# Optimization experiments

Hardware: AMD Instinct MI355X
Metric: run time of the kernel (lower is better)

## Reference

```python
import jax, jax.numpy as jnp
import numpy as np

N_NODES = 50000
D_FEAT = 128
N_EDGES = 600000
HIDDEN_1 = 128
HIDDEN_2 = 64


def setup_inputs() -> dict:
    key = jax.random.key(0)
    ks = jax.random.split(key, 8)
    features = jax.random.normal(ks[0], (N_NODES, D_FEAT), dtype=jnp.float32)
    edges = jax.random.randint(ks[1], (N_EDGES, 2), 0, N_NODES, dtype=jnp.int64)
    s1 = 1.0 / np.sqrt(D_FEAT)
    s2 = 1.0 / np.sqrt(2 * HIDDEN_1)
    s3 = 1.0 / np.sqrt(HIDDEN_2)
    return {
        "features": features,
        "edges": edges,
        "W_nb": jax.random.normal(ks[2], (D_FEAT, HIDDEN_1), dtype=jnp.float32) * s1,
        "b_nb": jnp.zeros((HIDDEN_1,), dtype=jnp.float32),
        "W_self": jax.random.normal(ks[3], (D_FEAT, HIDDEN_1), dtype=jnp.float32) * s1,
        "b_self": jnp.zeros((HIDDEN_1,), dtype=jnp.float32),
        "W_att1": jax.random.normal(ks[4], (2 * HIDDEN_1, HIDDEN_2), dtype=jnp.float32) * s2,
        "b_att1": jnp.zeros((HIDDEN_2,), dtype=jnp.float32),
        "W_att2": jax.random.normal(ks[5], (HIDDEN_2, 1), dtype=jnp.float32) * s3,
        "b_att2": jnp.zeros((1,), dtype=jnp.float32),
    }


def reference(features, edges, W_nb, b_nb, W_self, b_self, W_att1, b_att1, W_att2, b_att2):
    # gather endpoint node features for each edge: [E, D_FEAT]
    f1 = features[edges[:, 0]]
    f2 = features[edges[:, 1]]
    # per-endpoint dense projections with relu (inference: no dropout)
    h1 = jax.nn.relu(f1 @ W_nb + b_nb)      # [E, H1]
    h2 = jax.nn.relu(f2 @ W_self + b_self)  # [E, H1]
    h = jnp.concatenate([h1, h2], axis=1)   # [E, 2*H1]
    h = jax.nn.relu(h @ W_att1 + b_att1)    # [E, H2]
    weight = h @ W_att2 + b_att2            # [E, 1], linear output
    return weight
```

## Files before the change

kernel.cpp:

```cpp
#include <hip/hip_runtime.h>


#define N_NODES 50000
#define D_FEAT  128
#define H1      128
#define H2      64
#define N_EDGES 600000

typedef unsigned short u16;
typedef _Float16 f16;
typedef __attribute__((ext_vector_type(8))) _Float16 f16x8;
typedef __attribute__((ext_vector_type(2))) _Float16 f16x2;
typedef __attribute__((ext_vector_type(2))) float f32x2;
typedef __attribute__((ext_vector_type(4))) float f32x4;

union FragH { uint4 u; f16x8 v; };
union H2U   { unsigned u; f16x2 h; };

static __device__ __forceinline__ u16 f2h(float f) {
    union { f16 h; u16 u; } v; v.h = (f16)f; return v.u;
}
static __device__ __forceinline__ unsigned hpack(float a, float b) {
    return (unsigned)f2h(a) | ((unsigned)f2h(b) << 16);
}

__global__ __launch_bounds__(256) void prep_kernel(
    const float* __restrict__ Wnb, const float* __restrict__ Wsf,
    const float* __restrict__ Wat1,
    u16* __restrict__ W1F, u16* __restrict__ W2F)
{
    const int t = threadIdx.x;
    const int b = blockIdx.x;
    if (b < 16) {
        const int cs = b;
        const int kc = t >> 6, q = (t >> 4) & 3, m = t & 15;
        const int col = cs * 16 + m;
        const float* src = (col < H1) ? (Wnb + col) : (Wsf + (col - H1));
        const int k0 = kc * 32 + q * 8;
        float e[8];
        #pragma unroll
        for (int j = 0; j < 8; ++j) e[j] = src[(size_t)(k0 + j) * H1];
        uint4 pk = make_uint4(hpack(e[0], e[1]), hpack(e[2], e[3]),
                              hpack(e[4], e[5]), hpack(e[6], e[7]));
        *((uint4*)&W1F[((cs * 4 + kc) * 64 + q * 16 + m) * 8]) = pk;
    } else {
        for (int i = t; i < 4 * 8 * 64; i += 256) {
            const int lane = i & 63, pair = i >> 6;
            const int q = lane >> 4, m = lane & 15;
            const int cs2 = pair >> 3, kc = pair & 7;
            const int col2 = cs2 * 16 + m;
            const int k0 = kc * 32 + q * 8;
            float e[8];
            #pragma unroll
            for (int j = 0; j < 8; ++j) e[j] = Wat1[(size_t)(k0 + j) * H2 + col2];
            uint4 pk = make_uint4(hpack(e[0], e[1]), hpack(e[2], e[3]),
                                  hpack(e[4], e[5]), hpack(e[6], e[7]));
            *((uint4*)&W2F[(pair * 64 + lane) * 8]) = pk;
        }
    }
}

__global__ __launch_bounds__(256) void node_kernel(
    const float* __restrict__ feat,
    const u16* __restrict__ W1F,  const u16* __restrict__ W2F,
    const float* __restrict__ bnb,  const float* __restrict__ bsf,
    const float* __restrict__ bat1,
    u16* __restrict__ a1, u16* __restrict__ a2)
{
    __shared__ u16 Abuf[4 * 4 * 64 * 8];
    __shared__ u16 Hbuf[4 * 8 * 64 * 8];

    const int t    = threadIdx.x;
    const int w    = t >> 6;
    const int lane = t & 63;
    const int m    = lane & 15;
    const int q    = lane >> 4;
    const int n0   = blockIdx.x * 64;

    {
        const int kcs = t >> 6;
        const int k0  = kcs * 32 + q * 8;
        #pragma unroll
        for (int it = 0; it < 4; ++it) {
            const int gn = n0 + it * 16 + m;
            float4 va = make_float4(0.f,0.f,0.f,0.f), vb = va;
            if (gn < N_NODES) {
                const float* src = feat + (size_t)gn * D_FEAT + k0;
                va = *((const float4*)src);
                vb = *((const float4*)(src + 4));
            }
            uint4 pk = make_uint4(hpack(va.x, va.y), hpack(va.z, va.w),
                                  hpack(vb.x, vb.y), hpack(vb.z, vb.w));
            *((uint4*)&Abuf[(((it * 4 + kcs) * 64) + (t & 63)) * 8]) = pk;
        }
    }

    FragH w1f[4][4];
    #pragma unroll
    for (int ms = 0; ms < 4; ++ms)
        #pragma unroll
        for (int kc = 0; kc < 4; ++kc)
            w1f[ms][kc].u = *((const uint4*)&W1F[(((w * 4 + ms) * 4 + kc) * 64 + lane) * 8]);

    f32x4 acc1[4][4];
    #pragma unroll
    for (int i = 0; i < 4; ++i)
        #pragma unroll
        for (int j = 0; j < 4; ++j)
            acc1[i][j] = (f32x4){0.f, 0.f, 0.f, 0.f};

    __syncthreads();

    #pragma unroll
    for (int kc = 0; kc < 4; ++kc) {
        #pragma unroll
        for (int ns = 0; ns < 4; ++ns) {
            FragH ff; ff.u = *((const uint4*)&Abuf[((ns * 4 + kc) * 64 + lane) * 8]);
            #pragma unroll
            for (int ms = 0; ms < 4; ++ms)
                acc1[ms][ns] = __builtin_amdgcn_mfma_f32_16x16x32_f16(
                    w1f[ms][kc].v, ff.v, acc1[ms][ns], 0, 0, 0);
        }
    }

    #pragma unroll
    for (int ms = 0; ms < 4; ++ms) {
        const int hcol0 = w * 64 + ms * 16 + q * 4;
        const float* bsrc = (hcol0 < H1) ? (bnb + hcol0) : (bsf + (hcol0 - H1));
        const float4 bb = *((const float4*)bsrc);
        const int kc2 = hcol0 >> 5;
        const int q2  = (hcol0 >> 3) & 3;
        const int j0  = hcol0 & 7;
        #pragma unroll
        for (int ns = 0; ns < 4; ++ns) {
            const f32x4 a = acc1[ms][ns];
            const float v0 = fmaxf(a.x + bb.x, 0.f);
            const float v1 = fmaxf(a.y + bb.y, 0.f);
            const float v2 = fmaxf(a.z + bb.z, 0.f);
            const float v3 = fmaxf(a.w + bb.w, 0.f);
            const int idx = ((ns * 8 + kc2) * 64 + (q2 * 16 + m)) * 8 + j0;
            uint2 p; p.x = hpack(v0, v1); p.y = hpack(v2, v3);
            *((uint2*)&Hbuf[idx]) = p;
        }
    }

    FragH w2f[2][4];
    #pragma unroll
    for (int ns2 = 0; ns2 < 2; ++ns2) {
        const int cs2 = (w & 1) * 2 + ns2;
        #pragma unroll
        for (int kcl = 0; kcl < 4; ++kcl) {
            const int kc = kcl + ((w < 2) ? 0 : 4);
            w2f[ns2][kcl].u = *((const uint4*)&W2F[((cs2 * 8 + kc) * 64 + lane) * 8]);
        }
    }

    f32x4 acc2[4][2];
    #pragma unroll
    for (int i = 0; i < 4; ++i) { acc2[i][0] = (f32x4){0.f,0.f,0.f,0.f};
                                  acc2[i][1] = (f32x4){0.f,0.f,0.f,0.f}; }

    __syncthreads();

    #pragma unroll
    for (int kcl = 0; kcl < 4; ++kcl) {
        const int kc2 = kcl + ((w < 2) ? 0 : 4);
        #pragma unroll
        for (int ms = 0; ms < 4; ++ms) {
            FragH hf; hf.u = *((const uint4*)&Hbuf[((ms * 8 + kc2) * 64 + lane) * 8]);
            #pragma unroll
            for (int ns2 = 0; ns2 < 2; ++ns2)
                acc2[ms][ns2] = __builtin_amdgcn_mfma_f32_16x16x32_f16(
                    w2f[ns2][kcl].v, hf.v, acc2[ms][ns2], 0, 0, 0);
        }
    }

    u16* aout = (w < 2) ? a1 : a2;
    const int colbase = (w & 1) * 32;
    #pragma unroll
    for (int ns2 = 0; ns2 < 2; ++ns2) {
        const int c0 = colbase + ns2 * 16 + q * 4;
        float4 b2 = make_float4(0.f, 0.f, 0.f, 0.f);
        if (w < 2) b2 = *((const float4*)(bat1 + c0));
        #pragma unroll
        for (int ms = 0; ms < 4; ++ms) {
            const int node = n0 + ms * 16 + m;
            if (node < N_NODES) {
                const f32x4 a = acc2[ms][ns2];
                ushort4 pk;
                pk.x = f2h(a.x + b2.x); pk.y = f2h(a.y + b2.y);
                pk.z = f2h(a.z + b2.z); pk.w = f2h(a.w + b2.w);
                *((ushort4*)(aout + (size_t)node * H2 + c0)) = pk;
            }
        }
    }
}

static __device__ __forceinline__ float edot(uint4 a, uint4 b,
                                             float4 w0, float4 w1) {
    const f16x2 z = (f16x2)(f16)0;
    float s = 0.f;
    {
        H2U x, y; x.u = a.x; y.u = b.x;
        f16x2 r = __builtin_elementwise_max(x.h + y.h, z);
        f32x2 f = __builtin_convertvector(r, f32x2);
        s = fmaf(f.x, w0.x, fmaf(f.y, w0.y, s));
    }
    {
        H2U x, y; x.u = a.y; y.u = b.y;
        f16x2 r = __builtin_elementwise_max(x.h + y.h, z);
        f32x2 f = __builtin_convertvector(r, f32x2);
        s = fmaf(f.x, w0.z, fmaf(f.y, w0.w, s));
    }
    {
        H2U x, y; x.u = a.z; y.u = b.z;
        f16x2 r = __builtin_elementwise_max(x.h + y.h, z);
        f32x2 f = __builtin_convertvector(r, f32x2);
        s = fmaf(f.x, w1.x, fmaf(f.y, w1.y, s));
    }
    {
        H2U x, y; x.u = a.w; y.u = b.w;
        f16x2 r = __builtin_elementwise_max(x.h + y.h, z);
        f32x2 f = __builtin_convertvector(r, f32x2);
        s = fmaf(f.x, w1.z, fmaf(f.y, w1.w, s));
    }
    return s;
}

__global__ __launch_bounds__(256) void edge_kernel(
    const int* __restrict__ edges,
    const u16* __restrict__ a1, const u16* __restrict__ a2,
    const float* __restrict__ Wat2, const float* __restrict__ bat2,
    float* __restrict__ out)
{
    const int t = threadIdx.x;
    const int l = t & 7;
    const int g = t >> 3;
    const int base = blockIdx.x * 128 + g;

    const float4 w0 = ((const float4*)Wat2)[l * 2 + 0];
    const float4 w1 = ((const float4*)Wat2)[l * 2 + 1];
    const float  bias = bat2[0];

    int  e[4]; bool v[4]; int2 ep[4];
    #pragma unroll
    for (int i = 0; i < 4; ++i) {
        e[i] = base + i * 32;
        v[i] = e[i] < N_EDGES;
        ep[i] = v[i] ? ((const int2*)edges)[e[i]] : make_int2(0, 0);
    }

    uint4 q1[4], q2[4];
    #pragma unroll
    for (int i = 0; i < 4; ++i) {
        q1[i] = ((const uint4*)(a1 + (size_t)ep[i].x * H2))[l];
        q2[i] = ((const uint4*)(a2 + (size_t)ep[i].y * H2))[l];
    }

    float s[4];
    #pragma unroll
    for (int i = 0; i < 4; ++i) {
        s[i] = edot(q1[i], q2[i], w0, w1);
        s[i] += __shfl_down(s[i], 4, 8);
        s[i] += __shfl_down(s[i], 2, 8);
        s[i] += __shfl_down(s[i], 1, 8);
    }

    if (l == 0) {
        #pragma unroll
        for (int i = 0; i < 4; ++i)
            if (v[i]) out[e[i]] = s[i] + bias;
    }
}

extern "C" void kernel_launch(void* const* d_in, const int* in_sizes, int n_in,
                              void* d_out, int out_size, void* d_ws, size_t ws_size,
                              hipStream_t stream) {
    const float* feat  = (const float*)d_in[0];
    const int*   edges = (const int*)d_in[1];
    const float* Wnb   = (const float*)d_in[2];
    const float* bnb   = (const float*)d_in[3];
    const float* Wsf   = (const float*)d_in[4];
    const float* bsf   = (const float*)d_in[5];
    const float* Wat1  = (const float*)d_in[6];
    const float* bat1  = (const float*)d_in[7];
    const float* Wat2  = (const float*)d_in[8];
    const float* bat2  = (const float*)d_in[9];
    float* out = (float*)d_out;

    u16* a1  = (u16*)d_ws;
    u16* a2  = a1 + (size_t)N_NODES * H2;
    u16* W1F = a2 + (size_t)N_NODES * H2;
    u16* W2F = W1F + 16 * 4 * 64 * 8;

    prep_kernel<<<17, 256, 0, stream>>>(Wnb, Wsf, Wat1, W1F, W2F);

    const int node_blocks = (N_NODES + 63) / 64;
    node_kernel<<<node_blocks, 256, 0, stream>>>(feat, W1F, W2F,
                                                 bnb, bsf, bat1, a1, a2);

    const int edge_blocks = (N_EDGES + 127) / 128;
    edge_kernel<<<edge_blocks, 256, 0, stream>>>(edges, a1, a2, Wat2, bat2, out);
}
```

Before: 123.4 us.

## Load node features straight into MFMA fragments and widen edge work per group

```diff
diff --git a/kernel.cpp b/kernel.cpp
--- a/kernel.cpp
+++ b/kernel.cpp
@@ -11,6 +11,7 @@
 typedef _Float16 f16;
 typedef __attribute__((ext_vector_type(8))) _Float16 f16x8;
 typedef __attribute__((ext_vector_type(2))) _Float16 f16x2;
+typedef __attribute__((ext_vector_type(2))) __fp16 fp16x2_b;
 typedef __attribute__((ext_vector_type(2))) float f32x2;
 typedef __attribute__((ext_vector_type(4))) float f32x4;
 
@@ -22,6 +23,11 @@
 }
 static __device__ __forceinline__ unsigned hpack(float a, float b) {
     return (unsigned)f2h(a) | ((unsigned)f2h(b) << 16);
+}
+static __device__ __forceinline__ unsigned pkrtz(float a, float b) {
+    union { fp16x2_b h; unsigned u; } v;
+    v.h = __builtin_amdgcn_cvt_pkrtz(a, b);
+    return v.u;
 }
 
 __global__ __launch_bounds__(256) void prep_kernel(
@@ -67,7 +73,6 @@
     const float* __restrict__ bat1,
     u16* __restrict__ a1, u16* __restrict__ a2)
 {
-    __shared__ u16 Abuf[4 * 4 * 64 * 8];
     __shared__ u16 Hbuf[4 * 8 * 64 * 8];
 
     const int t    = threadIdx.x;
@@ -77,50 +82,42 @@
     const int q    = lane >> 4;
     const int n0   = blockIdx.x * 64;
 
-    {
-        const int kcs = t >> 6;
-        const int k0  = kcs * 32 + q * 8;
-        #pragma unroll
-        for (int it = 0; it < 4; ++it) {
-            const int gn = n0 + it * 16 + m;
+    FragH w1f[4][4];
+    #pragma unroll
+    for (int ms = 0; ms < 4; ++ms)
+        #pragma unroll
+        for (int kc = 0; kc < 4; ++kc)
+            w1f[ms][kc].u = *((const uint4*)&W1F[(((w * 4 + ms) * 4 + kc) * 64 + lane) * 8]);
+
+    f32x4 acc1[4][4];
+    #pragma unroll
+    for (int i = 0; i < 4; ++i)
+        #pragma unroll
+        for (int j = 0; j < 4; ++j)
+            acc1[i][j] = (f32x4){0.f, 0.f, 0.f, 0.f};
+
+    #pragma unroll
+    for (int kc = 0; kc < 4; ++kc) {
+        const int koff = kc * 32 + q * 8;
+        FragH ff[4];
+        #pragma unroll
+        for (int ns = 0; ns < 4; ++ns) {
+            const int gn = n0 + ns * 16 + m;
             float4 va = make_float4(0.f,0.f,0.f,0.f), vb = va;
             if (gn < N_NODES) {
-                const float* src = feat + (size_t)gn * D_FEAT + k0;
-                va = *((const float4*)src);
-                vb = *((const float4*)(src + 4));
+                const float* src = feat + (size_t)gn * D_FEAT + koff;
+                va = ((const float4*)src)[0];
+                vb = ((const float4*)src)[1];
             }
-            uint4 pk = make_uint4(hpack(va.x, va.y), hpack(va.z, va.w),
-                                  hpack(vb.x, vb.y), hpack(vb.z, vb.w));
-            *((uint4*)&Abuf[(((it * 4 + kcs) * 64) + (t & 63)) * 8]) = pk;
-        }
-    }
-
-    FragH w1f[4][4];
-    #pragma unroll
-    for (int ms = 0; ms < 4; ++ms)
-        #pragma unroll
-        for (int kc = 0; kc < 4; ++kc)
-            w1f[ms][kc].u = *((const uint4*)&W1F[(((w * 4 + ms) * 4 + kc) * 64 + lane) * 8]);
-
-    f32x4 acc1[4][4];
-    #pragma unroll
-    for (int i = 0; i < 4; ++i)
-        #pragma unroll
-        for (int j = 0; j < 4; ++j)
-            acc1[i][j] = (f32x4){0.f, 0.f, 0.f, 0.f};
-
-    __syncthreads();
-
-    #pragma unroll
-    for (int kc = 0; kc < 4; ++kc) {
-        #pragma unroll
-        for (int ns = 0; ns < 4; ++ns) {
-            FragH ff; ff.u = *((const uint4*)&Abuf[((ns * 4 + kc) * 64 + lane) * 8]);
+            ff[ns].u = make_uint4(pkrtz(va.x, va.y), pkrtz(va.z, va.w),
+                                  pkrtz(vb.x, vb.y), pkrtz(vb.z, vb.w));
+        }
+        #pragma unroll
+        for (int ns = 0; ns < 4; ++ns)
             #pragma unroll
             for (int ms = 0; ms < 4; ++ms)
                 acc1[ms][ns] = __builtin_amdgcn_mfma_f32_16x16x32_f16(
-                    w1f[ms][kc].v, ff.v, acc1[ms][ns], 0, 0, 0);
-        }
+                    w1f[ms][kc].v, ff[ns].v, acc1[ms][ns], 0, 0, 0);
     }
 
     #pragma unroll
@@ -236,30 +233,28 @@
     const int t = threadIdx.x;
     const int l = t & 7;
     const int g = t >> 3;
-    const int base = blockIdx.x * 128 + g;
+    const int base = blockIdx.x * 256 + g * 8;
+    if (base >= N_EDGES) return;
 
     const float4 w0 = ((const float4*)Wat2)[l * 2 + 0];
     const float4 w1 = ((const float4*)Wat2)[l * 2 + 1];
     const float  bias = bat2[0];
 
-    int  e[4]; bool v[4]; int2 ep[4];
-    #pragma unroll
-    for (int i = 0; i < 4; ++i) {
-        e[i] = base + i * 32;
-        v[i] = e[i] < N_EDGES;
-        ep[i] = v[i] ? ((const int2*)edges)[e[i]] : make_int2(0, 0);
-    }
-
-    uint4 q1[4], q2[4];
-    #pragma unroll
-    for (int i = 0; i < 4; ++i) {
+    int2 ep[8];
+    #pragma unroll
+    for (int i = 0; i < 8; ++i)
+        ep[i] = ((const int2*)edges)[base + i];
+
+    uint4 q1[8], q2[8];
+    #pragma unroll
+    for (int i = 0; i < 8; ++i) {
         q1[i] = ((const uint4*)(a1 + (size_t)ep[i].x * H2))[l];
         q2[i] = ((const uint4*)(a2 + (size_t)ep[i].y * H2))[l];
     }
 
-    float s[4];
-    #pragma unroll
-    for (int i = 0; i < 4; ++i) {
+    float s[8];
+    #pragma unroll
+    for (int i = 0; i < 8; ++i) {
         s[i] = edot(q1[i], q2[i], w0, w1);
         s[i] += __shfl_down(s[i], 4, 8);
         s[i] += __shfl_down(s[i], 2, 8);
@@ -267,9 +262,10 @@
     }
 
     if (l == 0) {
-        #pragma unroll
-        for (int i = 0; i < 4; ++i)
-            if (v[i]) out[e[i]] = s[i] + bias;
+        float4 o0 = make_float4(s[0]+bias, s[1]+bias, s[2]+bias, s[3]+bias);
+        float4 o1 = make_float4(s[4]+bias, s[5]+bias, s[6]+bias, s[7]+bias);
+        *((float4*)(out + base))     = o0;
+        *((float4*)(out + base + 4)) = o1;
     }
 }
 
@@ -299,6 +295,6 @@
     node_kernel<<<node_blocks, 256, 0, stream>>>(feat, W1F, W2F,
                                                  bnb, bsf, bat1, a1, a2);
 
-    const int edge_blocks = (N_EDGES + 127) / 128;
+    const int edge_blocks = (N_EDGES + 255) / 256;
     edge_kernel<<<edge_blocks, 256, 0, stream>>>(edges, a1, a2, Wat2, bat2, out);
 }
```

Measured after the change: 128.7 us. 4.3% more time.
